# Performance work log

Measured on AMD Instinct MI355X. Metric: run time of the kernel, lower is better.

## Reference

```python
import jax, jax.numpy as jnp
import numpy as np

B, DIM, HEADS, AGENT = 32, 768, 12, 49
H0 = W0 = 28
N = H0 * W0


def setup_inputs() -> dict:
    key = jax.random.key(0)
    ks = jax.random.split(key, 24)
    p = lambda i, shape: jax.random.normal(ks[i], shape, jnp.float32) * 0.02
    return {
        "rgb_fea": jax.random.normal(ks[0], (B, N, DIM), jnp.float32),
        "depth_fea": jax.random.normal(ks[1], (B, N, DIM), jnp.float32),
        "rgb_q_w": p(2, (DIM, DIM)), "rgb_kv_w": p(3, (DIM, 2 * DIM)),
        "rgb_proj_w": p(4, (DIM, DIM)), "rgb_proj_b": jnp.zeros((DIM,), jnp.float32),
        "depth_q_w": p(5, (DIM, DIM)), "depth_kv_w": p(6, (DIM, 2 * DIM)),
        "depth_proj_w": p(7, (DIM, DIM)), "depth_proj_b": jnp.zeros((DIM,), jnp.float32),
        "rgb_dwc_w": p(8, (3, 3, 1, DIM)), "rgb_dwc_b": jnp.zeros((DIM,), jnp.float32),
        "depth_dwc_w": p(9, (3, 3, 1, DIM)), "depth_dwc_b": jnp.zeros((DIM,), jnp.float32),
        "rgb_an_bias": p(10, (HEADS, AGENT, 7, 7)), "rgb_na_bias": p(11, (HEADS, AGENT, 7, 7)),
        "rgb_ah_bias": p(12, (1, HEADS, AGENT, H0, 1)), "rgb_aw_bias": p(13, (1, HEADS, AGENT, 1, W0)),
        "rgb_ha_bias": p(14, (1, HEADS, H0, 1, AGENT)), "rgb_wa_bias": p(15, (1, HEADS, 1, W0, AGENT)),
        "depth_an_bias": p(16, (HEADS, AGENT, 7, 7)), "depth_na_bias": p(17, (HEADS, AGENT, 7, 7)),
        "depth_ah_bias": p(18, (1, HEADS, AGENT, H0, 1)), "depth_aw_bias": p(19, (1, HEADS, AGENT, 1, W0)),
        "depth_ha_bias": p(20, (1, HEADS, H0, 1, AGENT)), "depth_wa_bias": p(21, (1, HEADS, 1, W0, AGENT)),
        "H": H0, "W": W0,
    }


def _dwc(x, w, bias):
    # depthwise 3x3 conv, padding=1. x: [b,H,W,c], w: [3,3,1,c]
    y = jax.lax.conv_general_dilated(
        x, w, (1, 1), "SAME",
        dimension_numbers=("NHWC", "HWIO", "NHWC"),
        feature_group_count=x.shape[-1])
    return y + bias


def reference(rgb_fea, depth_fea, rgb_q_w, rgb_kv_w, rgb_proj_w, rgb_proj_b,
              depth_q_w, depth_kv_w, depth_proj_w, depth_proj_b,
              rgb_dwc_w, rgb_dwc_b, depth_dwc_w, depth_dwc_b,
              rgb_an_bias, rgb_na_bias, rgb_ah_bias, rgb_aw_bias, rgb_ha_bias, rgb_wa_bias,
              depth_an_bias, depth_na_bias, depth_ah_bias, depth_aw_bias, depth_ha_bias, depth_wa_bias,
              H, W):
    b, n, c = rgb_fea.shape
    heads = HEADS
    hd = c // heads
    scale = hd ** -0.5
    agent = AGENT
    ps = int(agent ** 0.5)  # 7x7 agent grid via adaptive avg pool (exact since H % ps == 0)

    rgb_q = rgb_fea @ rgb_q_w
    depth_q = depth_fea @ depth_q_w
    rgb_kv = (rgb_fea @ rgb_kv_w).reshape(b, n, 2, c)
    depth_kv = (depth_fea @ depth_kv_w).reshape(b, n, 2, c)

    heads_split = lambda t: t.reshape(b, -1, heads, hd).transpose(0, 2, 1, 3)  # [b,h,n,d]
    pool = lambda q: q.reshape(b, ps, H // ps, ps, W // ps, c).mean(axis=(2, 4)).reshape(b, agent, c)

    rgb_qh = heads_split(rgb_q)
    rgb_kh = heads_split(rgb_kv[:, :, 0])
    rgb_vh = heads_split(rgb_kv[:, :, 1])
    depth_qh = heads_split(depth_q)
    depth_kh = heads_split(depth_kv[:, :, 0])
    depth_vh = heads_split(depth_kv[:, :, 1])
    rgb_ah = heads_split(pool(rgb_q))      # [b,h,agent,d]
    depth_ah = heads_split(pool(depth_q))

    def pos_bias(an, ah_b, aw_b):
        # agent->native bias: interpolate 7x7 -> HxW (bilinear, half-pixel = torch align_corners=False)
        p1 = jax.image.resize(an, (heads, agent, H, W), method="linear").reshape(1, heads, agent, H * W)
        p2 = (ah_b + aw_b).reshape(1, heads, agent, H * W)
        return p1 + p2

    def ag_bias(na, ha_b, wa_b):
        # native->agent bias
        b1 = jax.image.resize(na, (heads, agent, H, W), method="linear").reshape(1, heads, agent, H * W).transpose(0, 1, 3, 2)
        b2 = (ha_b + wa_b).reshape(1, heads, H * W, agent)
        return b1 + b2

    rgb_pb = pos_bias(rgb_an_bias, rgb_ah_bias, rgb_aw_bias)
    depth_pb = pos_bias(depth_an_bias, depth_ah_bias, depth_aw_bias)

    # agent aggregation (cross-modal): depth agents attend to rgb k/v and vice versa
    depth_agent_attn = jax.nn.softmax(jnp.einsum("bhad,bhnd->bhan", depth_ah * scale, rgb_kh) + rgb_pb, axis=-1)
    depth_agent_v = jnp.einsum("bhan,bhnd->bhad", depth_agent_attn, rgb_vh)
    rgb_agent_attn = jax.nn.softmax(jnp.einsum("bhad,bhnd->bhan", rgb_ah * scale, depth_kh) + depth_pb, axis=-1)
    rgb_agent_v = jnp.einsum("bhan,bhnd->bhad", rgb_agent_attn, depth_vh)

    rgb_ab = ag_bias(rgb_na_bias, rgb_ha_bias, rgb_wa_bias)
    depth_ab = ag_bias(depth_na_bias, depth_ha_bias, depth_wa_bias)

    # agent broadcast: native queries attend to the other modality's agents
    rgb_q_attn = jax.nn.softmax(jnp.einsum("bhnd,bhad->bhna", rgb_qh * scale, depth_ah) + depth_ab, axis=-1)
    rgb_out = jnp.einsum("bhna,bhad->bhnd", rgb_q_attn, depth_agent_v)
    depth_q_attn = jax.nn.softmax(jnp.einsum("bhnd,bhad->bhna", depth_qh * scale, rgb_ah) + rgb_ab, axis=-1)
    depth_out = jnp.einsum("bhna,bhad->bhnd", depth_q_attn, rgb_agent_v)

    merge = lambda t: t.transpose(0, 2, 1, 3).reshape(b, n, c)
    rgb_out = merge(rgb_out) + _dwc(merge(rgb_vh).reshape(b, H, W, c), rgb_dwc_w, rgb_dwc_b).reshape(b, n, c)
    depth_out = merge(depth_out) + _dwc(merge(depth_vh).reshape(b, H, W, c), depth_dwc_w, depth_dwc_b).reshape(b, n, c)

    rgb_out = rgb_out @ rgb_proj_w + rgb_proj_b
    depth_out = depth_out @ depth_proj_w + depth_proj_b
    return rgb_out, depth_out
```

## Files before the change

kernel.cpp:

```cpp
#include <hip/hip_runtime.h>
#include <hip/hip_bf16.h>

#define BATCH 32
#define NPOS 784
#define DIM 768
#define HEADS 12
#define HD 64
#define AGENT 49
#define HH 28
#define WW 28
#define MROWS (BATCH*NPOS)
#define SCALE 0.125f

using bf16 = __hip_bfloat16;
typedef __attribute__((ext_vector_type(4))) float f32x4;
typedef __attribute__((ext_vector_type(8))) short short8v;

__device__ __forceinline__ float bf2f(bf16 x) { return __bfloat162float(x); }
__device__ __forceinline__ float bfs2f(short s) {
    unsigned int u = ((unsigned int)(unsigned short)s) << 16;
    return __uint_as_float(u);
}
__device__ __forceinline__ unsigned short f2bf(float x) {
    unsigned int u = __float_as_uint(x);
    unsigned int r = (u + 0x7fffu + ((u >> 16) & 1u)) >> 16;
    return (unsigned short)r;
}

#define GLOAD_LDS16(g, l) __builtin_amdgcn_global_load_lds( \
    (const __attribute__((address_space(1))) unsigned int*)(g), \
    (__attribute__((address_space(3))) unsigned int*)(l), 16, 0, 0)

__global__ __launch_bounds__(256) void convert_bf16_2(
    const float* __restrict__ src0, bf16* __restrict__ dst0,
    const float* __restrict__ src1, bf16* __restrict__ dst1, int n8)
{
    int idx = blockIdx.x * 256 + threadIdx.x;
    if (idx >= 2 * n8) return;
    int sel = idx >= n8;
    int li = idx - sel * n8;
    const float* p = (sel ? src1 : src0) + (size_t)li * 8;
    float4 r0 = *reinterpret_cast<const float4*>(p);
    float4 r1 = *reinterpret_cast<const float4*>(p + 4);
    short8v v;
    v[0] = (short)f2bf(r0.x); v[1] = (short)f2bf(r0.y);
    v[2] = (short)f2bf(r0.z); v[3] = (short)f2bf(r0.w);
    v[4] = (short)f2bf(r1.x); v[5] = (short)f2bf(r1.y);
    v[6] = (short)f2bf(r1.z); v[7] = (short)f2bf(r1.w);
    *reinterpret_cast<short8v*>((short*)(sel ? dst1 : dst0) + (size_t)li * 8) = v;
}

__global__ __launch_bounds__(256) void transpose_w_bf16_2(
    const float* __restrict__ W0, bf16* __restrict__ Wt0,
    const float* __restrict__ W1, bf16* __restrict__ Wt1, int K, int N)
{
    __shared__ float t[32][33];
    int gyh = gridDim.y >> 1;
    int sel = blockIdx.y >= gyh;
    const float* W = sel ? W1 : W0;
    bf16* Wt = sel ? Wt1 : Wt0;
    int tx = threadIdx.x & 31, ty = threadIdx.x >> 5;
    int k0 = (blockIdx.y - sel * gyh) * 32, n0 = blockIdx.x * 32;
#pragma unroll
    for (int i = 0; i < 4; ++i)
        t[ty + 8 * i][tx] = W[(size_t)(k0 + ty + 8 * i) * N + n0 + tx];
    __syncthreads();
#pragma unroll
    for (int i = 0; i < 4; ++i)
        Wt[(size_t)(n0 + ty + 8 * i) * K + k0 + tx] = __float2bfloat16(t[tx][ty + 8 * i]);
}

template<bool OUTF32>
__global__ __launch_bounds__(256) void gemm_mfma(
    const bf16* __restrict__ A0, const bf16* __restrict__ Bt0,
    const float* __restrict__ bias0, void* __restrict__ Cp0,
    const bf16* __restrict__ A1, const bf16* __restrict__ Bt1,
    const float* __restrict__ bias1, void* __restrict__ Cp1,
    int M, int N, int K)
{
    __shared__ __align__(16) short As[128 * 64];
    __shared__ __align__(16) short Bs[128 * 64];

    int tid = threadIdx.x;
    int wave = tid >> 6, lane = tid & 63;

    int gx = gridDim.x;
    int gyh = gridDim.y >> 1;
    int nwg = gx * gridDim.y;
    int bid = blockIdx.y * gx + blockIdx.x;
    int cpx = nwg >> 3;
    int nb = (bid & 7) * cpx + (bid >> 3);
    int rowblk = nb / gx;
    int prob = rowblk >= gyh;
    int m0 = (rowblk - prob * gyh) * 128, n0 = (nb % gx) * 128;

    const short* Ab  = (const short*)(prob ? A1 : A0);
    const short* Btb = (const short*)(prob ? Bt1 : Bt0);
    const float* bias = prob ? bias1 : bias0;
    void* Cp = prob ? Cp1 : Cp0;

    int wm = (wave >> 1) * 64, wn = (wave & 1) * 64;
    int acol = lane & 15, kgrp = lane >> 4;

    f32x4 acc[4][4] = {};

    for (int k0 = 0; k0 < K; k0 += 64) {
#pragma unroll
        for (int it = 0; it < 4; ++it) {
            int idx = tid + 256 * it;
            int row = idx >> 3, seg = idx & 7;
            int sseg = seg ^ (row & 7);
            GLOAD_LDS16(Ab + (size_t)(m0 + row) * K + k0 + sseg * 8, &As[idx * 8]);
        }
#pragma unroll
        for (int it = 0; it < 4; ++it) {
            int idx = tid + 256 * it;
            int row = idx >> 3, seg = idx & 7;
            int sseg = seg ^ (row & 7);
            GLOAD_LDS16(Btb + (size_t)(n0 + row) * K + k0 + sseg * 8, &Bs[idx * 8]);
        }
        __syncthreads();

#pragma unroll
        for (int kk = 0; kk < 2; ++kk) {
            short8v af[4], bfr[4];
#pragma unroll
            for (int mf = 0; mf < 4; ++mf) {
                int row = wm + mf * 16 + acol;
                int seg = (kk * 4 + kgrp) ^ (row & 7);
                af[mf] = *reinterpret_cast<const short8v*>(&As[row * 64 + seg * 8]);
            }
#pragma unroll
            for (int nf = 0; nf < 4; ++nf) {
                int row = wn + nf * 16 + acol;
                int seg = (kk * 4 + kgrp) ^ (row & 7);
                bfr[nf] = *reinterpret_cast<const short8v*>(&Bs[row * 64 + seg * 8]);
            }
#pragma unroll
            for (int mf = 0; mf < 4; ++mf)
#pragma unroll
                for (int nf = 0; nf < 4; ++nf)
                    acc[mf][nf] = __builtin_amdgcn_mfma_f32_16x16x32_bf16(
                        af[mf], bfr[nf], acc[mf][nf], 0, 0, 0);
        }
        __syncthreads();
    }

    int rgrp = kgrp * 4, cidx = acol;
#pragma unroll
    for (int mf = 0; mf < 4; ++mf)
#pragma unroll
        for (int nf = 0; nf < 4; ++nf)
#pragma unroll
            for (int r = 0; r < 4; ++r) {
                int row = m0 + wm + mf * 16 + rgrp + r;
                int col = n0 + wn + nf * 16 + cidx;
                float v = acc[mf][nf][r];
                if constexpr (OUTF32)
                    ((float*)Cp)[(size_t)row * N + col] = v + bias[col];
                else
                    ((bf16*)Cp)[(size_t)row * N + col] = __float2bfloat16(v);
            }
}

__global__ void pool_kernel_2(const bf16* __restrict__ q0, float* __restrict__ ahp0,
                              const bf16* __restrict__ q1, float* __restrict__ ahp1)
{
    int idx = blockIdx.x * 256 + threadIdx.x;
    int tot = BATCH * AGENT * DIM;
    if (idx >= 2 * tot) return;
    int sel = idx >= tot;
    int li = idx - sel * tot;
    const bf16* q = sel ? q1 : q0;
    float* ahp = sel ? ahp1 : ahp0;
    int c = li % DIM;
    int a = (li / DIM) % AGENT;
    int b = li / (DIM * AGENT);
    int ai = a / 7, aj = a % 7;
    float s = 0.f;
#pragma unroll
    for (int u = 0; u < 4; ++u)
#pragma unroll
        for (int v = 0; v < 4; ++v) {
            int n = (ai * 4 + u) * WW + (aj * 4 + v);
            s += bf2f(q[((size_t)b * NPOS + n) * DIM + c]);
        }
    ahp[li] = s * (1.f / 16.f);
}

__device__ __forceinline__ float bilerp7(const float* __restrict__ img, int i, int j)
{
    float si = 0.25f * i - 0.375f, sj = 0.25f * j - 0.375f;
    int i0 = (int)floorf(si); float fi = si - i0;
    int j0 = (int)floorf(sj); float fj = sj - j0;
    int i0c = min(max(i0, 0), 6), i1c = min(max(i0 + 1, 0), 6);
    int j0c = min(max(j0, 0), 6), j1c = min(max(j0 + 1, 0), 6);
    float v00 = img[i0c * 7 + j0c], v01 = img[i0c * 7 + j1c];
    float v10 = img[i1c * 7 + j0c], v11 = img[i1c * 7 + j1c];
    return (1.f - fi) * ((1.f - fj) * v00 + fj * v01) + fi * ((1.f - fj) * v10 + fj * v11);
}

__global__ void pos_bias_kernel_2(
    const float* __restrict__ an0, const float* __restrict__ ah_b0,
    const float* __restrict__ aw_b0, bf16* __restrict__ pb0,
    const float* __restrict__ an1, const float* __restrict__ ah_b1,
    const float* __restrict__ aw_b1, bf16* __restrict__ pb1)
{
    int idx = blockIdx.x * 256 + threadIdx.x;
    int tot = HEADS * AGENT * NPOS;
    if (idx >= 2 * tot) return;
    int sel = idx >= tot;
    int li = idx - sel * tot;
    const float* an = sel ? an1 : an0;
    const float* ah_b = sel ? ah_b1 : ah_b0;
    const float* aw_b = sel ? aw_b1 : aw_b0;
    bf16* pb = sel ? pb1 : pb0;
    int n = li % NPOS;
    int a = (li / NPOS) % AGENT;
    int h = li / (NPOS * AGENT);
    int i = n / WW, j = n % WW;
    float v = bilerp7(an + (size_t)(h * AGENT + a) * 49, i, j);
    v += ah_b[(h * AGENT + a) * HH + i] + aw_b[(h * AGENT + a) * WW + j];
    pb[li] = __float2bfloat16(v);
}

__global__ void ag_bias_kernel_2(
    const float* __restrict__ na0, const float* __restrict__ ha_b0,
    const float* __restrict__ wa_b0, bf16* __restrict__ ab0,
    const float* __restrict__ na1, const float* __restrict__ ha_b1,
    const float* __restrict__ wa_b1, bf16* __restrict__ ab1)
{
    int idx = blockIdx.x * 256 + threadIdx.x;
    int tot = HEADS * NPOS * AGENT;
    if (idx >= 2 * tot) return;
    int sel = idx >= tot;
    int li = idx - sel * tot;
    const float* na = sel ? na1 : na0;
    const float* ha_b = sel ? ha_b1 : ha_b0;
    const float* wa_b = sel ? wa_b1 : wa_b0;
    bf16* ab = sel ? ab1 : ab0;
    int a = li % AGENT;
    int n = (li / AGENT) % NPOS;
    int h = li / (AGENT * NPOS);
    int i = n / WW, j = n % WW;
    float v = bilerp7(na + (size_t)(h * AGENT + a) * 49, i, j);
    v += ha_b[(h * HH + i) * AGENT + a] + wa_b[(h * WW + j) * AGENT + a];
    ab[li] = __float2bfloat16(v);
}

__global__ __launch_bounds__(256, 2) void agent_attn3(
    const float* __restrict__ ahp0, const bf16* __restrict__ kv0,
    const bf16* __restrict__ pb0, bf16* __restrict__ agent_v0,
    const float* __restrict__ ahp1, const bf16* __restrict__ kv1,
    const bf16* __restrict__ pb1, bf16* __restrict__ agent_v1)
{
    __shared__ __align__(16) char smem[75776];
    short (*pL)[64][72]  = (short (*)[64][72])smem;
    short (*VtL)[64][72] = (short (*)[64][72])(smem + 36864);
    float (*Om)[64][66]  = (float (*)[64][66])smem;
    float (*mw)[64]      = (float (*)[64])(smem + 73728);
    float (*lw)[64]      = (float (*)[64])(smem + 74752);

    int sel = blockIdx.x >= BATCH * HEADS;
    int blk = blockIdx.x - sel * BATCH * HEADS;
    const float* ahp = sel ? ahp1 : ahp0;
    const bf16* kv = sel ? kv1 : kv0;
    const bf16* pb = sel ? pb1 : pb0;
    bf16* agent_v = sel ? agent_v1 : agent_v0;

    int tid = threadIdx.x;
    int wave = tid >> 6, lane = tid & 63;
    int acol = lane & 15, kgrp = lane >> 4;
    int h = blk % HEADS;
    int b = blk / HEADS;
    const short* kvs = (const short*)kv;
    const bf16* pbh = pb + (size_t)h * AGENT * NPOS;

    short8v qa[2][4];
#pragma unroll
    for (int ks = 0; ks < 2; ++ks)
#pragma unroll
        for (int mf = 0; mf < 4; ++mf) {
            int a = mf * 16 + acol;
            short8v v = {};
            if (a < AGENT) {
                const float* src = ahp + ((size_t)b * AGENT + a) * DIM + h * HD + ks * 32 + kgrp * 8;
                float4 r0 = *reinterpret_cast<const float4*>(src);
                float4 r1 = *reinterpret_cast<const float4*>(src + 4);
                v[0] = (short)f2bf(r0.x * SCALE); v[1] = (short)f2bf(r0.y * SCALE);
                v[2] = (short)f2bf(r0.z * SCALE); v[3] = (short)f2bf(r0.w * SCALE);
                v[4] = (short)f2bf(r1.x * SCALE); v[5] = (short)f2bf(r1.y * SCALE);
                v[6] = (short)f2bf(r1.z * SCALE); v[7] = (short)f2bf(r1.w * SCALE);
            }
            qa[ks][mf] = v;
        }

    float mrun[16], lrun[16];
#pragma unroll
    for (int i = 0; i < 16; ++i) { mrun[i] = -1e30f; lrun[i] = 0.f; }
    f32x4 accO[4][4] = {};

    for (int t = wave; t < 13; t += 4) {
        int n0 = t * 64;
        {
            int p = lane & 31, dh = lane >> 5;
            const short* v0p = kvs + (size_t)(b * NPOS + n0 + 2 * p) * (2 * DIM) + DIM + h * HD + dh * 32;
#pragma unroll
            for (int s = 0; s < 4; ++s) {
                short8v va = {}, vb = {};
                if (n0 + 2 * p < NPOS)     va = *reinterpret_cast<const short8v*>(v0p + s * 8);
                if (n0 + 2 * p + 1 < NPOS) vb = *reinterpret_cast<const short8v*>(v0p + 2 * DIM + s * 8);
#pragma unroll
                for (int u = 0; u < 8; ++u) {
                    int d = dh * 32 + s * 8 + u;
                    unsigned int w = ((unsigned int)(unsigned short)va[u]) |
                                     (((unsigned int)(unsigned short)vb[u]) << 16);
                    *reinterpret_cast<unsigned int*>(&VtL[wave][d][2 * p]) = w;
                }
            }
        }

        short8v kb[2][4];
#pragma unroll
        for (int nf = 0; nf < 4; ++nf) {
            int n = n0 + nf * 16 + acol;
            bool val = (n < NPOS);
            const short* kp = kvs + (size_t)(b * NPOS + n) * (2 * DIM) + h * HD + kgrp * 8;
#pragma unroll
            for (int ks = 0; ks < 2; ++ks) {
                short8v v = {};
                if (val) v = *reinterpret_cast<const short8v*>(kp + ks * 32);
                kb[ks][nf] = v;
            }
        }

        f32x4 accS[4][4] = {};
#pragma unroll
        for (int mf = 0; mf < 4; ++mf)
#pragma unroll
            for (int nf = 0; nf < 4; ++nf) {
                accS[mf][nf] = __builtin_amdgcn_mfma_f32_16x16x32_bf16(qa[0][mf], kb[0][nf], accS[mf][nf], 0, 0, 0);
                accS[mf][nf] = __builtin_amdgcn_mfma_f32_16x16x32_bf16(qa[1][mf], kb[1][nf], accS[mf][nf], 0, 0, 0);
            }

#pragma unroll
        for (int mf = 0; mf < 4; ++mf)
#pragma unroll
            for (int r = 0; r < 4; ++r) {
                int a = mf * 16 + kgrp * 4 + r;
                float s[4];
                float mt = -1e30f;
#pragma unroll
                for (int nf = 0; nf < 4; ++nf) {
                    int n = n0 + nf * 16 + acol;
                    float sv = -1e30f;
                    if (n < NPOS) {
                        sv = accS[mf][nf][r];
                        if (a < AGENT) sv += bf2f(pbh[(size_t)a * NPOS + n]);
                    }
                    s[nf] = sv;
                    mt = fmaxf(mt, sv);
                }
#pragma unroll
                for (int off = 1; off < 16; off <<= 1)
                    mt = fmaxf(mt, __shfl_xor(mt, off));
                float mnew = fmaxf(mrun[mf * 4 + r], mt);
                float fac = __expf(mrun[mf * 4 + r] - mnew);
                float ps = 0.f;
#pragma unroll
                for (int nf = 0; nf < 4; ++nf) {
                    float pv = (s[nf] > -1e29f) ? __expf(s[nf] - mnew) : 0.f;
                    ps += pv;
                    pL[wave][a][nf * 16 + acol] = (short)f2bf(pv);
                }
#pragma unroll
                for (int off = 1; off < 16; off <<= 1)
                    ps += __shfl_xor(ps, off);
                mrun[mf * 4 + r] = mnew;
                lrun[mf * 4 + r] = lrun[mf * 4 + r] * fac + ps;
#pragma unroll
                for (int df = 0; df < 4; ++df) accO[mf][df][r] *= fac;
            }

        short8v vb2[2][4];
#pragma unroll
        for (int ks = 0; ks < 2; ++ks)
#pragma unroll
            for (int df = 0; df < 4; ++df)
                vb2[ks][df] = *reinterpret_cast<const short8v*>(
                    &VtL[wave][df * 16 + acol][ks * 32 + kgrp * 8]);
#pragma unroll
        for (int mf = 0; mf < 4; ++mf) {
#pragma unroll
            for (int ks = 0; ks < 2; ++ks) {
                short8v pa = *reinterpret_cast<const short8v*>(
                    &pL[wave][mf * 16 + acol][ks * 32 + kgrp * 8]);
#pragma unroll
                for (int df = 0; df < 4; ++df)
                    accO[mf][df] = __builtin_amdgcn_mfma_f32_16x16x32_bf16(pa, vb2[ks][df], accO[mf][df], 0, 0, 0);
            }
        }
    }

    if (acol == 0) {
#pragma unroll
        for (int mf = 0; mf < 4; ++mf)
#pragma unroll
            for (int r = 0; r < 4; ++r) {
                mw[wave][mf * 16 + kgrp * 4 + r] = mrun[mf * 4 + r];
                lw[wave][mf * 16 + kgrp * 4 + r] = lrun[mf * 4 + r];
            }
    }
    __syncthreads();
#pragma unroll
    for (int mf = 0; mf < 4; ++mf)
#pragma unroll
        for (int df = 0; df < 4; ++df)
#pragma unroll
            for (int r = 0; r < 4; ++r)
                Om[wave][mf * 16 + kgrp * 4 + r][df * 16 + acol] = accO[mf][df][r];
    __syncthreads();

    for (int idx = tid; idx < AGENT * HD; idx += 256) {
        int a = idx >> 6, d = idx & 63;
        float m = fmaxf(fmaxf(mw[0][a], mw[1][a]), fmaxf(mw[2][a], mw[3][a]));
        float l = 0.f, o = 0.f;
#pragma unroll
        for (int w = 0; w < 4; ++w) {
            float f = __expf(mw[w][a] - m);
            l += f * lw[w][a];
            o += f * Om[w][a][d];
        }
        ((short*)agent_v)[(((size_t)b * HEADS + h) * AGENT + a) * HD + d] = (short)f2bf(o / l);
    }
}

__global__ __launch_bounds__(256) void q_attn_mfma(
    bf16* qpre0, const bf16* __restrict__ kv_own0,
    const float* __restrict__ ahp_x0, const bf16* __restrict__ ab_x0,
    const bf16* __restrict__ agv_x0,
    const float* __restrict__ dwc_w0, const float* __restrict__ dwc_b0,
    bf16* qpre1, const bf16* __restrict__ kv_own1,
    const float* __restrict__ ahp_x1, const bf16* __restrict__ ab_x1,
    const bf16* __restrict__ agv_x1,
    const float* __restrict__ dwc_w1, const float* __restrict__ dwc_b1)
{
    __shared__ short pL[4][16][72];
    __shared__ float oL[4][16][68];
    __shared__ float wS[9][64];
    __shared__ float cbS[64];

    int sel = blockIdx.x >= BATCH * HEADS * 2;
    int blk = blockIdx.x - sel * BATCH * HEADS * 2;
    bf16* qpre = sel ? qpre1 : qpre0;
    const bf16* kv_own = sel ? kv_own1 : kv_own0;
    const float* ahp_x = sel ? ahp_x1 : ahp_x0;
    const bf16* ab_x = sel ? ab_x1 : ab_x0;
    const bf16* agv_x = sel ? agv_x1 : agv_x0;
    const float* dwc_w = sel ? dwc_w1 : dwc_w0;
    const float* dwc_b = sel ? dwc_b1 : dwc_b0;

    int half = blk & 1;
    int h = (blk >> 1) % HEADS;
    int b = blk / (2 * HEADS);
    int tid = threadIdx.x;
    int wave = tid >> 6, lane = tid & 63;
    int acol = lane & 15, kgrp = lane >> 4;

    for (int i = tid; i < 9 * 64; i += 256)
        wS[i >> 6][i & 63] = dwc_w[(i >> 6) * DIM + h * HD + (i & 63)];
    if (tid < 64) cbS[tid] = dwc_b[h * HD + tid];
    for (int i = tid; i < 4 * 16 * 72; i += 256)
        ((short*)pL)[i] = 0;

    short8v bs[2][4];
#pragma unroll
    for (int ks = 0; ks < 2; ++ks)
#pragma unroll
        for (int nf = 0; nf < 4; ++nf) {
            int a = nf * 16 + acol;
            short8v v = {};
            if (a < AGENT) {
                const float* src = ahp_x + ((size_t)b * AGENT + a) * DIM + h * HD + ks * 32 + kgrp * 8;
                float4 r0 = *reinterpret_cast<const float4*>(src);
                float4 r1 = *reinterpret_cast<const float4*>(src + 4);
                v[0] = (short)f2bf(r0.x * SCALE); v[1] = (short)f2bf(r0.y * SCALE);
                v[2] = (short)f2bf(r0.z * SCALE); v[3] = (short)f2bf(r0.w * SCALE);
                v[4] = (short)f2bf(r1.x * SCALE); v[5] = (short)f2bf(r1.y * SCALE);
                v[6] = (short)f2bf(r1.z * SCALE); v[7] = (short)f2bf(r1.w * SCALE);
            }
            bs[ks][nf] = v;
        }

    const short* agvs = (const short*)agv_x;
    short8v bv[2][4];
#pragma unroll
    for (int ks = 0; ks < 2; ++ks)
#pragma unroll
        for (int nf = 0; nf < 4; ++nf) {
            int d = nf * 16 + acol;
            short8v v = {};
#pragma unroll
            for (int i = 0; i < 8; ++i) {
                int a = ks * 32 + kgrp * 8 + i;
                if (a < AGENT)
                    v[i] = agvs[(((size_t)b * HEADS + h) * AGENT + a) * HD + d];
            }
            bv[ks][nf] = v;
        }

    __syncthreads();

    int tstart = half ? 25 : 0, tend = half ? 49 : 25;
    for (int t = tstart + wave; t < tend; t += 4) {
        int n0 = t * 16;
        const short* qrow = (const short*)qpre +
            ((size_t)(b * NPOS + n0 + acol)) * DIM + h * HD + kgrp * 8;
        short8v a0 = *reinterpret_cast<const short8v*>(qrow);
        short8v a1 = *reinterpret_cast<const short8v*>(qrow + 32);

        f32x4 accs[4] = {};
#pragma unroll
        for (int nf = 0; nf < 4; ++nf) {
            accs[nf] = __builtin_amdgcn_mfma_f32_16x16x32_bf16(a0, bs[0][nf], accs[nf], 0, 0, 0);
            accs[nf] = __builtin_amdgcn_mfma_f32_16x16x32_bf16(a1, bs[1][nf], accs[nf], 0, 0, 0);
        }

        float inv[4];
#pragma unroll
        for (int r = 0; r < 4; ++r) {
            int n = n0 + kgrp * 4 + r;
            float sarr[4];
            float m = -1e30f;
#pragma unroll
            for (int nf = 0; nf < 4; ++nf) {
                int a = nf * 16 + acol;
                float s = -1e30f;
                if (a < AGENT)
                    s = accs[nf][r] + bf2f(ab_x[((size_t)h * NPOS + n) * AGENT + a]);
                sarr[nf] = s;
                m = fmaxf(m, s);
            }
#pragma unroll
            for (int off = 1; off < 16; off <<= 1)
                m = fmaxf(m, __shfl_xor(m, off));
            float ls = 0.f;
#pragma unroll
            for (int nf = 0; nf < 4; ++nf) {
                float p = (sarr[nf] > -1e29f) ? __expf(sarr[nf] - m) : 0.f;
                sarr[nf] = p;
                ls += p;
            }
#pragma unroll
            for (int off = 1; off < 16; off <<= 1)
                ls += __shfl_xor(ls, off);
            inv[r] = 1.f / ls;
#pragma unroll
            for (int nf = 0; nf < 4; ++nf) {
                int a = nf * 16 + acol;
                if (a < AGENT)
                    pL[wave][kgrp * 4 + r][a] = (short)f2bf(sarr[nf]);
            }
        }

        short8v p0 = *reinterpret_cast<const short8v*>(&pL[wave][acol][kgrp * 8]);
        short8v p1 = *reinterpret_cast<const short8v*>(&pL[wave][acol][kgrp * 8 + 32]);

        f32x4 acco[4] = {};
#pragma unroll
        for (int nf = 0; nf < 4; ++nf) {
            acco[nf] = __builtin_amdgcn_mfma_f32_16x16x32_bf16(p0, bv[0][nf], acco[nf], 0, 0, 0);
            acco[nf] = __builtin_amdgcn_mfma_f32_16x16x32_bf16(p1, bv[1][nf], acco[nf], 0, 0, 0);
        }

#pragma unroll
        for (int r = 0; r < 4; ++r)
#pragma unroll
            for (int nf = 0; nf < 4; ++nf)
                oL[wave][kgrp * 4 + r][nf * 16 + acol] = acco[nf][r] * inv[r];

#pragma unroll
        for (int it2 = 0; it2 < 2; ++it2) {
            int item = lane + 64 * it2;
            int rl = item >> 3, d8 = item & 7;
            int n = n0 + rl;
            int i = n / WW, j = n % WW;
            float accv[8];
            {
                float4 o0 = *reinterpret_cast<const float4*>(&oL[wave][rl][d8 * 8]);
                float4 o1 = *reinterpret_cast<const float4*>(&oL[wave][rl][d8 * 8 + 4]);
                accv[0] = o0.x + cbS[d8 * 8 + 0]; accv[1] = o0.y + cbS[d8 * 8 + 1];
                accv[2] = o0.z + cbS[d8 * 8 + 2]; accv[3] = o0.w + cbS[d8 * 8 + 3];
                accv[4] = o1.x + cbS[d8 * 8 + 4]; accv[5] = o1.y + cbS[d8 * 8 + 5];
                accv[6] = o1.z + cbS[d8 * 8 + 6]; accv[7] = o1.w + cbS[d8 * 8 + 7];
            }
#pragma unroll
            for (int di = -1; di <= 1; ++di) {
                int ii = i + di;
                if (ii < 0 || ii >= HH) continue;
#pragma unroll
                for (int dj = -1; dj <= 1; ++dj) {
                    int jj = j + dj;
                    if (jj < 0 || jj >= WW) continue;
                    short8v vv = *reinterpret_cast<const short8v*>(
                        (const short*)kv_own + ((size_t)(b * NPOS + ii * WW + jj)) * (2 * DIM) + DIM + h * HD + d8 * 8);
                    int tap = (di + 1) * 3 + (dj + 1);
#pragma unroll
                    for (int u = 0; u < 8; ++u)
                        accv[u] += wS[tap][d8 * 8 + u] * bfs2f(vv[u]);
                }
            }
            short8v ov;
#pragma unroll
            for (int u = 0; u < 8; ++u) ov[u] = (short)f2bf(accv[u]);
            *reinterpret_cast<short8v*>((short*)qpre +
                ((size_t)(b * NPOS + n)) * DIM + h * HD + d8 * 8) = ov;
        }
    }
}

extern "C" void kernel_launch(void* const* d_in, const int* in_sizes, int n_in,
                              void* d_out, int out_size, void* d_ws, size_t ws_size,
                              hipStream_t stream)
{
    const float* rgb_fea    = (const float*)d_in[0];
    const float* depth_fea  = (const float*)d_in[1];
    const float* rgb_q_w    = (const float*)d_in[2];
    const float* rgb_kv_w   = (const float*)d_in[3];
    const float* rgb_proj_w = (const float*)d_in[4];
    const float* rgb_proj_b = (const float*)d_in[5];
    const float* depth_q_w    = (const float*)d_in[6];
    const float* depth_kv_w   = (const float*)d_in[7];
    const float* depth_proj_w = (const float*)d_in[8];
    const float* depth_proj_b = (const float*)d_in[9];
    const float* rgb_dwc_w   = (const float*)d_in[10];
    const float* rgb_dwc_b   = (const float*)d_in[11];
    const float* depth_dwc_w = (const float*)d_in[12];
    const float* depth_dwc_b = (const float*)d_in[13];
    const float* rgb_an   = (const float*)d_in[14];
    const float* rgb_na   = (const float*)d_in[15];
    const float* rgb_ah_b = (const float*)d_in[16];
    const float* rgb_aw_b = (const float*)d_in[17];
    const float* rgb_ha_b = (const float*)d_in[18];
    const float* rgb_wa_b = (const float*)d_in[19];
    const float* depth_an   = (const float*)d_in[20];
    const float* depth_na   = (const float*)d_in[21];
    const float* depth_ah_b = (const float*)d_in[22];
    const float* depth_aw_b = (const float*)d_in[23];
    const float* depth_ha_b = (const float*)d_in[24];
    const float* depth_wa_b = (const float*)d_in[25];

    char* ws = (char*)d_ws;
    size_t off = 0;
    auto alloc = [&](size_t bytes) -> void* {
        void* p = ws + off;
        off += (bytes + 255) & ~(size_t)255;
        return p;
    };
    bf16* rgb_q    = (bf16*)alloc((size_t)MROWS * DIM * 2);
    bf16* depth_q  = (bf16*)alloc((size_t)MROWS * DIM * 2);
    bf16* rgb_kv   = (bf16*)alloc((size_t)MROWS * 2 * DIM * 2);
    bf16* depth_kv = (bf16*)alloc((size_t)MROWS * 2 * DIM * 2);
    bf16* rgb_pb    = (bf16*)alloc((size_t)HEADS * AGENT * NPOS * 2);
    bf16* depth_pb  = (bf16*)alloc((size_t)HEADS * AGENT * NPOS * 2);
    bf16* rgb_ab    = (bf16*)alloc((size_t)HEADS * NPOS * AGENT * 2);
    bf16* depth_ab  = (bf16*)alloc((size_t)HEADS * NPOS * AGENT * 2);
    bf16* rgb_agv   = (bf16*)alloc((size_t)BATCH * HEADS * AGENT * HD * 2);
    bf16* depth_agv = (bf16*)alloc((size_t)BATCH * HEADS * AGENT * HD * 2);
    bf16* proj_wt_r = (bf16*)alloc((size_t)DIM * DIM * 2);
    bf16* proj_wt_d = (bf16*)alloc((size_t)DIM * DIM * 2);
    size_t ubase = off;
    bf16* q_wt_r  = (bf16*)alloc((size_t)DIM * DIM * 2);
    bf16* kv_wt_r = (bf16*)alloc((size_t)DIM * 2 * DIM * 2);
    bf16* q_wt_d  = (bf16*)alloc((size_t)DIM * DIM * 2);
    bf16* kv_wt_d = (bf16*)alloc((size_t)DIM * 2 * DIM * 2);
    off = ubase;
    float* rgb_ahp   = (float*)alloc((size_t)BATCH * AGENT * DIM * 4);
    float* depth_ahp = (float*)alloc((size_t)BATCH * AGENT * DIM * 4);

    bf16* fea_bf_r = (bf16*)d_out;
    bf16* fea_bf_d = fea_bf_r + (size_t)MROWS * DIM;

    dim3 blk(256);
    int n8 = MROWS * DIM / 8;

    convert_bf16_2<<<(2 * n8 + 255) / 256, blk, 0, stream>>>(rgb_fea, fea_bf_r, depth_fea, fea_bf_d, n8);
    transpose_w_bf16_2<<<dim3(24, 48), blk, 0, stream>>>(rgb_q_w, q_wt_r, depth_q_w, q_wt_d, DIM, DIM);
    transpose_w_bf16_2<<<dim3(48, 48), blk, 0, stream>>>(rgb_kv_w, kv_wt_r, depth_kv_w, kv_wt_d, DIM, 2 * DIM);
    transpose_w_bf16_2<<<dim3(24, 48), blk, 0, stream>>>(rgb_proj_w, proj_wt_r, depth_proj_w, proj_wt_d, DIM, DIM);

    gemm_mfma<false><<<dim3(6, 392), blk, 0, stream>>>(
        fea_bf_r, q_wt_r, nullptr, rgb_q,
        fea_bf_d, q_wt_d, nullptr, depth_q, MROWS, DIM, DIM);
    gemm_mfma<false><<<dim3(12, 392), blk, 0, stream>>>(
        fea_bf_r, kv_wt_r, nullptr, rgb_kv,
        fea_bf_d, kv_wt_d, nullptr, depth_kv, MROWS, 2 * DIM, DIM);

    pool_kernel_2<<<(2 * BATCH * AGENT * DIM + 255) / 256, blk, 0, stream>>>(
        rgb_q, rgb_ahp, depth_q, depth_ahp);

    pos_bias_kernel_2<<<(2 * HEADS * AGENT * NPOS + 255) / 256, blk, 0, stream>>>(
        rgb_an, rgb_ah_b, rgb_aw_b, rgb_pb,
        depth_an, depth_ah_b, depth_aw_b, depth_pb);
    ag_bias_kernel_2<<<(2 * HEADS * NPOS * AGENT + 255) / 256, blk, 0, stream>>>(
        rgb_na, rgb_ha_b, rgb_wa_b, rgb_ab,
        depth_na, depth_ha_b, depth_wa_b, depth_ab);

    agent_attn3<<<2 * BATCH * HEADS, blk, 0, stream>>>(
        depth_ahp, rgb_kv, rgb_pb, depth_agv,
        rgb_ahp, depth_kv, depth_pb, rgb_agv);

    q_attn_mfma<<<2 * BATCH * HEADS * 2, blk, 0, stream>>>(
        rgb_q, rgb_kv, depth_ahp, depth_ab, depth_agv, rgb_dwc_w, rgb_dwc_b,
        depth_q, depth_kv, rgb_ahp, rgb_ab, rgb_agv, depth_dwc_w, depth_dwc_b);

    float* out = (float*)d_out;
    gemm_mfma<true><<<dim3(6, 392), blk, 0, stream>>>(
        rgb_q, proj_wt_r, rgb_proj_b, out,
        depth_q, proj_wt_d, depth_proj_b, out + (size_t)MROWS * DIM, MROWS, DIM, DIM);
}
```

Baseline: 697.0 us.

## Split depthwise conv out of q-attention into LDS-tiled standalone kernel

Moves the 3x3 depthwise conv from the q_attn_mfma epilogue into a separate kernel. The new kernel stages a 6-row by 28-column by 128-channel halo tile of V in shared memory, so each V element is read from global memory once rather than once per tap. The attention kernel now writes its bf16 output without the conv. The cost is an extra kernel launch and an extra read-modify-write of the q output buffer.

```diff
diff --git a/kernel.cpp b/kernel.cpp
--- a/kernel.cpp
+++ b/kernel.cpp
@@ -11,6 +11,8 @@
 #define WW 28
 #define MROWS (BATCH*NPOS)
 #define SCALE 0.125f
+#define CONV_CG 6
+#define CONV_IG 7
 
 using bf16 = __hip_bfloat16;
 typedef __attribute__((ext_vector_type(4))) float f32x4;
@@ -436,29 +438,20 @@
 }
 
 __global__ __launch_bounds__(256) void q_attn_mfma(
-    bf16* qpre0, const bf16* __restrict__ kv_own0,
-    const float* __restrict__ ahp_x0, const bf16* __restrict__ ab_x0,
+    bf16* qpre0, const float* __restrict__ ahp_x0, const bf16* __restrict__ ab_x0,
     const bf16* __restrict__ agv_x0,
-    const float* __restrict__ dwc_w0, const float* __restrict__ dwc_b0,
-    bf16* qpre1, const bf16* __restrict__ kv_own1,
-    const float* __restrict__ ahp_x1, const bf16* __restrict__ ab_x1,
-    const bf16* __restrict__ agv_x1,
-    const float* __restrict__ dwc_w1, const float* __restrict__ dwc_b1)
+    bf16* qpre1, const float* __restrict__ ahp_x1, const bf16* __restrict__ ab_x1,
+    const bf16* __restrict__ agv_x1)
 {
     __shared__ short pL[4][16][72];
     __shared__ float oL[4][16][68];
-    __shared__ float wS[9][64];
-    __shared__ float cbS[64];
 
     int sel = blockIdx.x >= BATCH * HEADS * 2;
     int blk = blockIdx.x - sel * BATCH * HEADS * 2;
     bf16* qpre = sel ? qpre1 : qpre0;
-    const bf16* kv_own = sel ? kv_own1 : kv_own0;
     const float* ahp_x = sel ? ahp_x1 : ahp_x0;
     const bf16* ab_x = sel ? ab_x1 : ab_x0;
     const bf16* agv_x = sel ? agv_x1 : agv_x0;
-    const float* dwc_w = sel ? dwc_w1 : dwc_w0;
-    const float* dwc_b = sel ? dwc_b1 : dwc_b0;
 
     int half = blk & 1;
     int h = (blk >> 1) % HEADS;
@@ -467,9 +460,6 @@
     int wave = tid >> 6, lane = tid & 63;
     int acol = lane & 15, kgrp = lane >> 4;
 
-    for (int i = tid; i < 9 * 64; i += 256)
-        wS[i >> 6][i & 63] = dwc_w[(i >> 6) * DIM + h * HD + (i & 63)];
-    if (tid < 64) cbS[tid] = dwc_b[h * HD + tid];
     for (int i = tid; i < 4 * 16 * 72; i += 256)
         ((short*)pL)[i] = 0;
 
@@ -584,38 +574,91 @@
             int item = lane + 64 * it2;
             int rl = item >> 3, d8 = item & 7;
             int n = n0 + rl;
-            int i = n / WW, j = n % WW;
-            float accv[8];
-            {
-                float4 o0 = *reinterpret_cast<const float4*>(&oL[wave][rl][d8 * 8]);
-                float4 o1 = *reinterpret_cast<const float4*>(&oL[wave][rl][d8 * 8 + 4]);
-                accv[0] = o0.x + cbS[d8 * 8 + 0]; accv[1] = o0.y + cbS[d8 * 8 + 1];
-                accv[2] = o0.z + cbS[d8 * 8 + 2]; accv[3] = o0.w + cbS[d8 * 8 + 3];
-                accv[4] = o1.x + cbS[d8 * 8 + 4]; accv[5] = o1.y + cbS[d8 * 8 + 5];
-                accv[6] = o1.z + cbS[d8 * 8 + 6]; accv[7] = o1.w + cbS[d8 * 8 + 7];
-            }
-#pragma unroll
-            for (int di = -1; di <= 1; ++di) {
-                int ii = i + di;
-                if (ii < 0 || ii >= HH) continue;
-#pragma unroll
-                for (int dj = -1; dj <= 1; ++dj) {
-                    int jj = j + dj;
-                    if (jj < 0 || jj >= WW) continue;
-                    short8v vv = *reinterpret_cast<const short8v*>(
-                        (const short*)kv_own + ((size_t)(b * NPOS + ii * WW + jj)) * (2 * DIM) + DIM + h * HD + d8 * 8);
-                    int tap = (di + 1) * 3 + (dj + 1);
-#pragma unroll
-                    for (int u = 0; u < 8; ++u)
-                        accv[u] += wS[tap][d8 * 8 + u] * bfs2f(vv[u]);
-                }
-            }
+            float4 o0 = *reinterpret_cast<const float4*>(&oL[wave][rl][d8 * 8]);
+            float4 o1 = *reinterpret_cast<const float4*>(&oL[wave][rl][d8 * 8 + 4]);
             short8v ov;
-#pragma unroll
-            for (int u = 0; u < 8; ++u) ov[u] = (short)f2bf(accv[u]);
+            ov[0] = (short)f2bf(o0.x); ov[1] = (short)f2bf(o0.y);
+            ov[2] = (short)f2bf(o0.z); ov[3] = (short)f2bf(o0.w);
+            ov[4] = (short)f2bf(o1.x); ov[5] = (short)f2bf(o1.y);
+            ov[6] = (short)f2bf(o1.z); ov[7] = (short)f2bf(o1.w);
             *reinterpret_cast<short8v*>((short*)qpre +
                 ((size_t)(b * NPOS + n)) * DIM + h * HD + d8 * 8) = ov;
         }
+    }
+}
+
+__global__ __launch_bounds__(256) void dwc_kernel(
+    bf16* pre0, const bf16* __restrict__ kv0,
+    const float* __restrict__ w0, const float* __restrict__ b0,
+    bf16* pre1, const bf16* __restrict__ kv1,
+    const float* __restrict__ w1, const float* __restrict__ b1)
+{
+    __shared__ __align__(16) short Vs[168][136];
+    __shared__ float wS[9][128];
+    __shared__ float cbS[128];
+
+    int blk = blockIdx.x;
+    int per = BATCH * CONV_CG * CONV_IG;
+    int sel = blk >= per;
+    blk -= sel * per;
+    bf16* pre = sel ? pre1 : pre0;
+    const short* kvs = (const short*)(sel ? kv1 : kv0);
+    const float* dw = sel ? w1 : w0;
+    const float* db = sel ? b1 : b0;
+
+    int ig = blk % CONV_IG;
+    int cg = (blk / CONV_IG) % CONV_CG;
+    int b  = blk / (CONV_IG * CONV_CG);
+    int c0 = cg * 128;
+    int tid = threadIdx.x;
+
+    for (int i = tid; i < 9 * 128; i += 256)
+        wS[i >> 7][i & 127] = dw[(i >> 7) * DIM + c0 + (i & 127)];
+    if (tid < 128) cbS[tid] = db[c0 + tid];
+
+    for (int it = 0; it < 11; ++it) {
+        int item = tid + 256 * it;
+        if (item >= 168 * 16) break;
+        int pos = item >> 4, c8 = item & 15;
+        int ii = pos / 28, jj = pos % 28;
+        int irow = ig * 4 - 1 + ii;
+        short8v v = {};
+        if (irow >= 0 && irow < HH)
+            v = *reinterpret_cast<const short8v*>(
+                kvs + (size_t)(b * NPOS + irow * WW + jj) * (2 * DIM) + DIM + c0 + c8 * 8);
+        *reinterpret_cast<short8v*>(&Vs[pos][c8 * 8]) = v;
+    }
+    __syncthreads();
+
+#pragma unroll
+    for (int it = 0; it < 7; ++it) {
+        int item = tid + 256 * it;
+        int opos = item >> 4, c8 = item & 15;
+        int oi = opos / 28, oj = opos % 28;
+        int n = (ig * 4 + oi) * WW + oj;
+        short* pp = (short*)pre + (size_t)(b * NPOS + n) * DIM + c0 + c8 * 8;
+        short8v pv = *reinterpret_cast<const short8v*>(pp);
+        float acc[8];
+#pragma unroll
+        for (int u = 0; u < 8; ++u) acc[u] = bfs2f(pv[u]) + cbS[c8 * 8 + u];
+#pragma unroll
+        for (int di = -1; di <= 1; ++di) {
+#pragma unroll
+            for (int dj = -1; dj <= 1; ++dj) {
+                int jj = oj + dj;
+                if (jj < 0 || jj >= WW) continue;
+                int pos = (oi + 1 + di) * 28 + jj;
+                short8v vv = *reinterpret_cast<const short8v*>(&Vs[pos][c8 * 8]);
+                int tap = (di + 1) * 3 + (dj + 1);
+#pragma unroll
+                for (int u = 0; u < 8; ++u)
+                    acc[u] += wS[tap][c8 * 8 + u] * bfs2f(vv[u]);
+            }
+        }
+        short8v ov;
+#pragma unroll
+        for (int u = 0; u < 8; ++u) ov[u] = (short)f2bf(acc[u]);
+        *reinterpret_cast<short8v*>(pp) = ov;
     }
 }
 
@@ -711,8 +754,12 @@
         rgb_ahp, depth_kv, depth_pb, rgb_agv);
 
     q_attn_mfma<<<2 * BATCH * HEADS * 2, blk, 0, stream>>>(
-        rgb_q, rgb_kv, depth_ahp, depth_ab, depth_agv, rgb_dwc_w, rgb_dwc_b,
-        depth_q, depth_kv, rgb_ahp, rgb_ab, rgb_agv, depth_dwc_w, depth_dwc_b);
+        rgb_q, depth_ahp, depth_ab, depth_agv,
+        depth_q, rgb_ahp, rgb_ab, rgb_agv);
+
+    dwc_kernel<<<2 * BATCH * CONV_CG * CONV_IG, blk, 0, stream>>>(
+        rgb_q, rgb_kv, rgb_dwc_w, rgb_dwc_b,
+        depth_q, depth_kv, depth_dwc_w, depth_dwc_b);
 
     float* out = (float*)d_out;
     gemm_mfma<true><<<dim3(6, 392), blk, 0, stream>>>(
```

New measurement: 683.4 us. Within noise of the previous version (-1.9%).
